# Performance work log

Measured on AMD Instinct MI355X. Metric: run time of the kernel, lower is better.

The kernel has to match this reference:

```python
import jax, jax.numpy as jnp
import numpy as np

B, T, C = 2, 2048, 1024
HS, DS = 8, 32      # short heads, short qk dim
HL, DL = 8, 128     # long heads, long qk dim
HD = 64             # value/output head dim = n_embd // n_head
WIN_S, WIN_L = 256, 1024
NEG = jnp.finfo(jnp.float32).min


def _window_mask(t, window):
    # additive mask: disallow future (i<j) and tokens older than the window
    i = jnp.arange(t)[:, None]
    j = jnp.arange(t)[None, :]
    bad = (i - j < 0) | (i - j >= window)
    return bad.astype(jnp.float32) * NEG  # [T,T]


def _attn(x, Wqk, Wv, n_h, d_qk, d_v, window):
    b, t, _ = x.shape
    qk = x @ Wqk                                      # [B,T,2*n_h*d_qk]
    q, k = jnp.split(qk, 2, axis=-1)
    q = q.reshape(b, t, n_h, d_qk).transpose(0, 2, 1, 3)  # [B,H,T,dqk]
    k = k.reshape(b, t, n_h, d_qk).transpose(0, 2, 1, 3)
    v = (x @ Wv).reshape(b, t, n_h, d_v).transpose(0, 2, 1, 3)  # [B,H,T,dv]
    scale = 1.0 / jnp.sqrt(jnp.float32(d_qk))
    scores = jnp.einsum('bhqd,bhkd->bhqk', q, k) * scale
    scores = scores + _window_mask(t, window)
    p = jax.nn.softmax(scores, axis=-1)
    return jnp.einsum('bhqk,bhkd->bhqd', p, v)        # [B,H,T,dv]


def setup_inputs() -> dict:
    key = jax.random.key(0)
    ks = jax.random.split(key, 6)
    s = 0.02
    return {
        'x': jax.random.normal(ks[0], (B, T, C), dtype=jnp.float32),
        'Wqk_short': jax.random.normal(ks[1], (C, 2 * HS * DS), dtype=jnp.float32) * s,
        'Wv_short': jax.random.normal(ks[2], (C, HS * HD), dtype=jnp.float32) * s,
        'Wqk_long': jax.random.normal(ks[3], (C, 2 * HL * DL), dtype=jnp.float32) * s,
        'Wv_long': jax.random.normal(ks[4], (C, HL * HD), dtype=jnp.float32) * s,
        'Wproj': jax.random.normal(ks[5], (C, C), dtype=jnp.float32) * s,
    }


def reference(x, Wqk_short, Wv_short, Wqk_long, Wv_long, Wproj):
    b, t, c = x.shape
    y_short = _attn(x, Wqk_short, Wv_short, HS, DS, HD, WIN_S)  # [B,HS,T,HD]
    y_long = _attn(x, Wqk_long, Wv_long, HL, DL, HD, WIN_L)     # [B,HL,T,HD]
    y = jnp.concatenate([y_short, y_long], axis=1)              # [B,H,T,HD]
    y = y.transpose(0, 2, 1, 3).reshape(b, t, c)
    return y @ Wproj
```

## Files before the change

kernel.cpp:

```cpp
#include <hip/hip_runtime.h>
#include <math.h>

#define B_    2
#define T_    2048
#define C_    1024
#define HS_   8
#define DS_   32
#define HL_   8
#define DL_   128
#define HD_   64
#define WINS_ 256
#define WINL_ 1024
#define NALL_ 3584

typedef __bf16 bf16x8 __attribute__((ext_vector_type(8)));
typedef float floatx4 __attribute__((ext_vector_type(4)));

__device__ __forceinline__ ushort f2bf(float f) {
    union { float f; unsigned u; } v; v.f = f;
    unsigned r = v.u + 0x7fff + ((v.u >> 16) & 1);
    return (ushort)(r >> 16);
}
__device__ __forceinline__ float bf2f(ushort u) {
    union { unsigned u; float f; } v; v.u = ((unsigned)u) << 16;
    return v.f;
}

#define DPP_STEP(x, ctrl, op)                                                \
    {                                                                        \
        float _t = __builtin_bit_cast(                                       \
            float, __builtin_amdgcn_update_dpp(                              \
                       0, __builtin_bit_cast(int, (x)), (ctrl), 0xf, 0xf,    \
                       true));                                               \
        (x) = op((x), _t);                                                   \
    }
__device__ __forceinline__ float dpp_max16(float x) {
    DPP_STEP(x, 0xB1, fmaxf);
    DPP_STEP(x, 0x4E, fmaxf);
    DPP_STEP(x, 0x141, fmaxf);
    DPP_STEP(x, 0x140, fmaxf);
    return x;
}
__device__ __forceinline__ float dpp_add16(float x) {
#define FADD_(a, b) ((a) + (b))
    DPP_STEP(x, 0xB1, FADD_);
    DPP_STEP(x, 0x4E, FADD_);
    DPP_STEP(x, 0x141, FADD_);
    DPP_STEP(x, 0x140, FADD_);
#undef FADD_
    return x;
}

__device__ __forceinline__ void gload_lds16(const void* g, void* l) {
    __builtin_amdgcn_global_load_lds(
        (const __attribute__((address_space(1))) void*)g,
        (__attribute__((address_space(3))) void*)l, 16, 0, 0);
}

__global__ __launch_bounds__(256) void prep(
    const float* __restrict__ x, ushort* __restrict__ x16,
    const float* __restrict__ Wqk_s, const float* __restrict__ Wv_s,
    const float* __restrict__ Wqk_l, const float* __restrict__ Wv_l,
    const float* __restrict__ Wproj, ushort* __restrict__ WallT,
    ushort* __restrict__ WprojT) {
    __shared__ float t[32][33];
    int bid = blockIdx.x;
    if (bid < 4096) {
        const int i = bid * 256 + threadIdx.x;
        float4 v = ((const float4*)x)[i];
        ushort4 o;
        o.x = f2bf(v.x); o.y = f2bf(v.y); o.z = f2bf(v.z); o.w = f2bf(v.w);
        ((ushort4*)x16)[i] = o;
        return;
    }
    bid -= 4096;
    const float* W; ushort* WT; int N, rowoff;
    if (bid < 512)       { W = Wqk_s; WT = WallT;  N = 512;  rowoff = 0; }
    else if (bid < 1024) { bid -= 512;  W = Wv_s;  WT = WallT;  N = 512;  rowoff = 512; }
    else if (bid < 3072) { bid -= 1024; W = Wqk_l; WT = WallT;  N = 2048; rowoff = 1024; }
    else if (bid < 3584) { bid -= 3072; W = Wv_l;  WT = WallT;  N = 512;  rowoff = 3072; }
    else                 { bid -= 3584; W = Wproj; WT = WprojT; N = 1024; rowoff = 0; }
    const int nt = N / 32;
    const int n0 = (bid % nt) * 32;
    const int k0 = (bid / nt) * 32;
    const int tx = threadIdx.x & 31;
    const int ty = threadIdx.x >> 5;
#pragma unroll
    for (int i = 0; i < 4; ++i)
        t[ty + 8 * i][tx] = W[(size_t)(k0 + ty + 8 * i) * N + n0 + tx];
    __syncthreads();
#pragma unroll
    for (int i = 0; i < 4; ++i)
        WT[(size_t)(rowoff + n0 + ty + 8 * i) * 1024 + k0 + tx] =
            f2bf(t[tx][ty + 8 * i]);
}

template <int BM, int BN, int TH, typename OT, bool FUSEV>
__global__ __launch_bounds__(TH, 4) void gemm_bf16(const ushort* __restrict__ A,
                                                   const ushort* __restrict__ BT,
                                                   OT* __restrict__ Cm,
                                                   ushort* __restrict__ VT,
                                                   int M, int N, int K) {
    __shared__ ushort S[3][(BM + BN) * 32];
    constexpr int WM = TH / 128;
    constexpr int NI = BM / WM / 16;
    constexpr int JB = BN / 32;
    constexpr int NLD = (BM + BN) * 4 / TH;

    const int tid = threadIdx.x;
    const int m0 = blockIdx.y * BM;
    const int n0 = blockIdx.x * BN;
    const int wave = tid >> 6;
    const int lane = tid & 63;
    const int wm = (wave >> 1) * (BM / WM);
    const int wn = (wave & 1) * (BN / 2);
    const int l15 = lane & 15;
    const int quad = lane >> 4;

    floatx4 acc[NI][JB] = {};

    const ushort* sbase[NLD];
#pragma unroll
    for (int i = 0; i < NLD; ++i) {
        const int idx = tid + TH * i;
        const int row = idx >> 2;
        const int ch = (idx & 3) * 8;
        sbase[i] = (row < BM) ? A + (size_t)(m0 + row) * K + ch
                              : BT + (size_t)(n0 + row - BM) * K + ch;
    }

#define STAGE(buf, kt)                                                      \
    {                                                                       \
        _Pragma("unroll") for (int i_ = 0; i_ < NLD; ++i_)                  \
            gload_lds16(sbase[i_] + (kt),                                   \
                        &S[buf][(wave * 64 + TH * i_) * 8]);                \
    }

#define COMPUTE(buf)                                                        \
    {                                                                       \
        bf16x8 af[NI], bfr[JB];                                             \
        _Pragma("unroll") for (int i = 0; i < NI; ++i) af[i] =              \
            *(const bf16x8*)&S[buf][(wm + i * 16 + l15) * 32 + quad * 8];   \
        _Pragma("unroll") for (int j = 0; j < JB; ++j) bfr[j] =             \
            *(const bf16x8*)&S[buf][(BM + wn + j * 16 + l15) * 32 +         \
                                    quad * 8];                              \
        _Pragma("unroll") for (int i = 0; i < NI; ++i)                      \
            _Pragma("unroll") for (int j = 0; j < JB; ++j) acc[i][j] =      \
                __builtin_amdgcn_mfma_f32_16x16x32_bf16(af[i], bfr[j],      \
                                                        acc[i][j], 0, 0, 0); \
    }

#define WAIT_CUR()                                                    \
    {                                                                 \
        if constexpr (NLD == 4)                                       \
            asm volatile("s_waitcnt vmcnt(4)" ::: "memory");          \
        else if constexpr (NLD == 3)                                  \
            asm volatile("s_waitcnt vmcnt(3)" ::: "memory");          \
        else                                                          \
            asm volatile("s_waitcnt vmcnt(2)" ::: "memory");          \
    }

    STAGE(0, 0);
    STAGE(1, 32);
    int cur = 0;
    for (int kt = 0; kt + 32 < K; kt += 32) {
        WAIT_CUR();
        __builtin_amdgcn_s_barrier();
        __builtin_amdgcn_sched_barrier(0);
        if (kt + 64 < K) {
            int nxt2 = cur + 2;
            if (nxt2 >= 3) nxt2 -= 3;
            STAGE(nxt2, kt + 64);
        }
        COMPUTE(cur);
        ++cur;
        if (cur == 3) cur = 0;
    }
    asm volatile("s_waitcnt vmcnt(0)" ::: "memory");
    __builtin_amdgcn_s_barrier();
    __builtin_amdgcn_sched_barrier(0);
    COMPUTE(cur);
#undef STAGE
#undef COMPUTE
#undef WAIT_CUR

    bool vtile = false;
    if constexpr (FUSEV)
        vtile = (n0 >= 512 && n0 < 1024) || (n0 >= 3072);

    if (FUSEV && vtile) {
#pragma unroll
        for (int i = 0; i < NI; ++i) {
            const int m = m0 + wm + i * 16 + quad * 4;
            const int bb = m >> 11;
            const int t = m & 2047;
#pragma unroll
            for (int j = 0; j < JB; ++j) {
                const int col = n0 + wn + j * 16 + l15;
                const int vcol = (col < 1024) ? (col - 512) : (col - 2560);
                ushort4 val;
                val.x = f2bf(acc[i][j][0]);
                val.y = f2bf(acc[i][j][1]);
                val.z = f2bf(acc[i][j][2]);
                val.w = f2bf(acc[i][j][3]);
                *(ushort4*)&VT[((size_t)(bb * 1024 + vcol)) * T_ + t] = val;
            }
        }
    } else {
#pragma unroll
        for (int i = 0; i < NI; ++i)
#pragma unroll
            for (int j = 0; j < JB; ++j)
#pragma unroll
                for (int r = 0; r < 4; ++r) {
                    const size_t idx =
                        (size_t)(m0 + wm + i * 16 + quad * 4 + r) * N + n0 +
                        wn + j * 16 + l15;
                    if constexpr (sizeof(OT) == 2)
                        Cm[idx] = f2bf(acc[i][j][r]);
                    else
                        Cm[idx] = acc[i][j][r];
                }
    }
}

template <int D, int WIN, bool SPLIT>
__device__ __forceinline__ void attn_dev(
    const ushort* __restrict__ act, const ushort* __restrict__ vt,
    ushort* __restrict__ y, ushort* __restrict__ po, float* __restrict__ pm,
    float* __restrict__ pl, float scale2, int qoff, int koff, int head_off,
    int h, int gh, int b, int t0, int zs, ushort* lds) {
    constexpr int STR = D + 8;
    constexpr int PSTR = 72;
    constexpr int NKS = D / 32;
    constexpr int QCH = D / 8;
    constexpr int NKLD = (64 * QCH) / 256;

    ushort* Ks = lds;
    ushort* VTs = Ks + 64 * STR;
    ushort* Ps = VTs + 64 * PSTR;

    const int tid = threadIdx.x;
    const int wave = tid >> 6;
    const int lane = tid & 63;
    const int l15 = lane & 15;
    const int quad = lane >> 4;
    const int qmin = t0 + wave * 16;

    int k0s = t0 - WIN + 1;
    if (k0s < 0) k0s = 0;
    k0s &= ~63;

    int ks_begin = k0s, ks_last = t0;
    if (SPLIT) {
        const int nt = ((t0 - k0s) >> 6) + 1;
        const int ntlo = (nt + 1) >> 1;
        if (zs == 0) {
            ks_last = k0s + (ntlo - 1) * 64;
        } else {
            if (ntlo >= nt) {
#pragma unroll
                for (int r = 0; r < 4; ++r) {
                    const int t = qmin + quad * 4 + r;
                    const size_t ridx =
                        (((size_t)(zs * 2 + b) * 8 + h) * T_ + t);
                    if (l15 == 0) { pm[ridx] = -1e30f; pl[ridx] = 0.f; }
#pragma unroll
                    for (int j = 0; j < 4; ++j)
                        po[ridx * 64 + j * 16 + l15] = 0;
                }
                return;
            }
            ks_begin = k0s + ntlo * 64;
        }
    }

    const ushort* qbase = act + (size_t)(b * T_ + t0) * NALL_ + qoff + h * D;
    const ushort* kbase = act + (size_t)(b * T_) * NALL_ + koff + h * D;
    const ushort* vtb = vt + (size_t)((b * 16 + gh) * HD_) * T_;

    int krow[NKLD], kch[NKLD];
#pragma unroll
    for (int i = 0; i < NKLD; ++i) {
        const int idx = tid + 256 * i;
        krow[i] = idx / QCH;
        kch[i] = idx % QCH;
    }
    const int vd0 = tid >> 3, vc0 = (tid & 7) * 8;
    const int vd1 = (tid + 256) >> 3, vc1 = ((tid + 256) & 7) * 8;

    int4 kreg[NKLD], vreg0, vreg1;
#pragma unroll
    for (int i = 0; i < NKLD; ++i)
        kreg[i] = *(const int4*)(kbase + (size_t)(ks_begin + krow[i]) * NALL_ +
                                 kch[i] * 8);
    vreg0 = *(const int4*)(vtb + (size_t)vd0 * T_ + ks_begin + vc0);
    vreg1 = *(const int4*)(vtb + (size_t)vd1 * T_ + ks_begin + vc1);

    for (int idx = tid; idx < 64 * QCH; idx += 256) {
        const int row = idx / QCH;
        const int ch = idx % QCH;
        *(int4*)&Ks[row * STR + ch * 8] =
            *(const int4*)(qbase + (size_t)row * NALL_ + ch * 8);
    }
    __syncthreads();
    bf16x8 qa[NKS];
#pragma unroll
    for (int ks = 0; ks < NKS; ++ks)
        qa[ks] = *(const bf16x8*)&Ks[(wave * 16 + l15) * STR + ks * 32 + quad * 8];

    float m_i[4], l_i[4];
    floatx4 o_acc[4] = {};
#pragma unroll
    for (int r = 0; r < 4; ++r) { m_i[r] = -1e30f; l_i[r] = 0.f; }

    for (int k0 = ks_begin; k0 <= ks_last; k0 += 64) {
        __syncthreads();
#pragma unroll
        for (int i = 0; i < NKLD; ++i)
            *(int4*)&Ks[krow[i] * STR + kch[i] * 8] = kreg[i];
        *(int4*)&VTs[vd0 * PSTR + vc0] = vreg0;
        *(int4*)&VTs[vd1 * PSTR + vc1] = vreg1;
        __syncthreads();
        if (k0 + 64 <= ks_last) {
#pragma unroll
            for (int i = 0; i < NKLD; ++i)
                kreg[i] = *(const int4*)(kbase +
                                         (size_t)(k0 + 64 + krow[i]) * NALL_ +
                                         kch[i] * 8);
            vreg0 = *(const int4*)(vtb + (size_t)vd0 * T_ + k0 + 64 + vc0);
            vreg1 = *(const int4*)(vtb + (size_t)vd1 * T_ + k0 + 64 + vc1);
        }

        floatx4 s[4] = {};
#pragma unroll
        for (int ks = 0; ks < NKS; ++ks) {
#pragma unroll
            for (int j = 0; j < 4; ++j) {
                const bf16x8 bb =
                    *(const bf16x8*)&Ks[(j * 16 + l15) * STR + ks * 32 + quad * 8];
                s[j] = __builtin_amdgcn_mfma_f32_16x16x32_bf16(qa[ks], bb, s[j],
                                                               0, 0, 0);
            }
        }

        const bool full = (k0 + 63 <= qmin) && ((qmin + 15) - k0 <= WIN - 1);
        if (full) {
#pragma unroll
            for (int j = 0; j < 4; ++j)
#pragma unroll
                for (int r = 0; r < 4; ++r) s[j][r] *= scale2;
        } else {
#pragma unroll
            for (int j = 0; j < 4; ++j) {
                const int kj = k0 + j * 16 + l15;
#pragma unroll
                for (int r = 0; r < 4; ++r) {
                    const int rel = (qmin + quad * 4 + r) - kj;
                    s[j][r] = (rel < 0 || rel >= WIN) ? -1e30f : s[j][r] * scale2;
                }
            }
        }

        float rm[4];
#pragma unroll
        for (int r = 0; r < 4; ++r) {
            float t = fmaxf(fmaxf(s[0][r], s[1][r]), fmaxf(s[2][r], s[3][r]));
            rm[r] = dpp_max16(t);
        }
        const bool need = (rm[0] > m_i[0] + 8.f) || (rm[1] > m_i[1] + 8.f) ||
                          (rm[2] > m_i[2] + 8.f) || (rm[3] > m_i[3] + 8.f);
        if (__any(need)) {
#pragma unroll
            for (int r = 0; r < 4; ++r) {
                const float mn = fmaxf(m_i[r], rm[r]);
                const float a = exp2f(m_i[r] - mn);
                m_i[r] = mn;
                l_i[r] *= a;
#pragma unroll
                for (int j = 0; j < 4; ++j) o_acc[j][r] *= a;
            }
        }
#pragma unroll
        for (int r = 0; r < 4; ++r) {
            float sum = 0.f;
#pragma unroll
            for (int j = 0; j < 4; ++j) {
                const float e = exp2f(s[j][r] - m_i[r]);
                sum += e;
                Ps[(wave * 16 + quad * 4 + r) * PSTR + j * 16 + l15] = f2bf(e);
            }
            sum = dpp_add16(sum);
            l_i[r] += sum;
        }

#pragma unroll
        for (int kks = 0; kks < 2; ++kks) {
            const bf16x8 pa =
                *(const bf16x8*)&Ps[(wave * 16 + l15) * PSTR + kks * 32 + quad * 8];
#pragma unroll
            for (int j = 0; j < 4; ++j) {
                const bf16x8 vb =
                    *(const bf16x8*)&VTs[(j * 16 + l15) * PSTR + kks * 32 + quad * 8];
                o_acc[j] = __builtin_amdgcn_mfma_f32_16x16x32_bf16(pa, vb, o_acc[j],
                                                                   0, 0, 0);
            }
        }
    }

    if (SPLIT) {
#pragma unroll
        for (int r = 0; r < 4; ++r) {
            const int t = qmin + quad * 4 + r;
            const size_t ridx = (((size_t)(zs * 2 + b) * 8 + h) * T_ + t);
            if (l15 == 0) { pm[ridx] = m_i[r]; pl[ridx] = l_i[r]; }
#pragma unroll
            for (int j = 0; j < 4; ++j)
                po[ridx * 64 + j * 16 + l15] = f2bf(o_acc[j][r]);
        }
    } else {
#pragma unroll
        for (int r = 0; r < 4; ++r) {
            const float inv = 1.f / l_i[r];
            ushort* yrow = y + (size_t)(b * T_ + qmin + quad * 4 + r) * C_ +
                           head_off + h * HD_;
#pragma unroll
            for (int j = 0; j < 4; ++j)
                yrow[j * 16 + l15] = f2bf(o_acc[j][r] * inv);
        }
    }
}

__global__ __launch_bounds__(256, 4) void attn_sched(
    const ushort* __restrict__ act, const ushort* __restrict__ vt,
    ushort* __restrict__ y, ushort* __restrict__ po, float* __restrict__ pm,
    float* __restrict__ pl) {
    extern __shared__ ushort smem[];
    int x = blockIdx.x;
    if (x < 1024) {
        const int zs = x & 1;
        const int b = (x >> 1) & 1;
        const int h = (x >> 2) & 7;
        const int t0 = (31 - (x >> 5)) * 64;
        attn_dev<DL_, WINL_, true>(act, vt, y, po, pm, pl,
                                   0.12752021352994164f,
                                   1024, 2048, 512, h, 8 + h, b, t0, zs, smem);
    } else {
        x -= 1024;
        const int b = x & 1;
        const int h = (x >> 1) & 7;
        const int t0 = (31 - (x >> 4)) * 64;
        attn_dev<DS_, WINS_, false>(act, vt, y, po, pm, pl,
                                    0.2550404270598833f,
                                    0, 256, 0, h, h, b, t0, 0, smem);
    }
}

__global__ __launch_bounds__(256) void combine(const ushort* __restrict__ po,
                                               const float* __restrict__ pm,
                                               const float* __restrict__ pl,
                                               ushort* __restrict__ y) {
    const int gid = blockIdx.x * 256 + threadIdx.x;
    const int row = gid >> 4;
    const int cg = (gid & 15) * 4;
    const int b = row >> 14;
    const int h = (row >> 11) & 7;
    const int t = row & 2047;

    const float m0 = pm[row], m1 = pm[32768 + row];
    const float l0 = pl[row], l1 = pl[32768 + row];
    const float m = fmaxf(m0, m1);
    const float e0 = exp2f(m0 - m);
    const float e1 = exp2f(m1 - m);
    const float inv = 1.f / (l0 * e0 + l1 * e1);

    const ushort4 o0 = *(const ushort4*)&po[(size_t)row * 64 + cg];
    const ushort4 o1 = *(const ushort4*)&po[((size_t)32768 + row) * 64 + cg];

    ushort4 r;
    r.x = f2bf((bf2f(o0.x) * e0 + bf2f(o1.x) * e1) * inv);
    r.y = f2bf((bf2f(o0.y) * e0 + bf2f(o1.y) * e1) * inv);
    r.z = f2bf((bf2f(o0.z) * e0 + bf2f(o1.z) * e1) * inv);
    r.w = f2bf((bf2f(o0.w) * e0 + bf2f(o1.w) * e1) * inv);
    *(ushort4*)&y[(size_t)(b * T_ + t) * C_ + 512 + h * 64 + cg] = r;
}

extern "C" void kernel_launch(void* const* d_in, const int* in_sizes, int n_in,
                              void* d_out, int out_size, void* d_ws,
                              size_t ws_size, hipStream_t stream) {
    const float* x         = (const float*)d_in[0];
    const float* Wqk_short = (const float*)d_in[1];
    const float* Wv_short  = (const float*)d_in[2];
    const float* Wqk_long  = (const float*)d_in[3];
    const float* Wv_long   = (const float*)d_in[4];
    const float* Wproj     = (const float*)d_in[5];
    float* out = (float*)d_out;

    const int M = B_ * T_;

    ushort* x16    = (ushort*)d_ws;
    ushort* WallT  = x16 + (size_t)M * C_;
    ushort* WprojT = WallT + (size_t)NALL_ * C_;
    ushort* yb16   = WprojT + (size_t)C_ * C_;
    ushort* act    = yb16 + (size_t)M * C_;
    ushort* vt     = act + (size_t)M * NALL_;
    ushort* po     = vt + (size_t)32 * HD_ * T_;
    float*  pm     = (float*)(po + (size_t)2 * 32768 * 64);
    float*  pl     = pm + (size_t)2 * 32768;

    dim3 blk(256);
    prep<<<dim3(8704), blk, 0, stream>>>(x, x16, Wqk_short, Wv_short, Wqk_long,
                                         Wv_long, Wproj, WallT, WprojT);

    gemm_bf16<256, 128, 512, ushort, true>
        <<<dim3(NALL_ / 128, M / 256), dim3(512), 0, stream>>>(
            x16, WallT, act, vt, M, NALL_, C_);

    const int attn_lds = (64 * (DL_ + 8) + 64 * 72 * 2) * 2;
    attn_sched<<<dim3(1536), blk, attn_lds, stream>>>(act, vt, yb16, po, pm, pl);

    combine<<<dim3(2048), blk, 0, stream>>>(po, pm, pl, yb16);

    gemm_bf16<64, 64, 256, float, false>
        <<<dim3(C_ / 64, M / 64), blk, 0, stream>>>(yb16, WprojT, out, nullptr,
                                                    M, C_, C_);
}
```

Before: 201.3 us.

## Use 128-query attention tiles with 8 waves sharing K/V loads

Each attention block now has 512 threads and covers 128 queries instead of 64, so every K/V tile staged in LDS is reused by twice as many waves and the grid is halved. Q fragments are now read straight from global memory into registers instead of being staged through LDS. The key range is extended by one tile to cover the larger query block. This raises per-block LDS and register demand and changes the split balance for the long heads.

```diff
diff --git a/kernel.cpp b/kernel.cpp
--- a/kernel.cpp
+++ b/kernel.cpp
@@ -231,14 +231,16 @@
     float* __restrict__ pl, float scale2, int qoff, int koff, int head_off,
     int h, int gh, int b, int t0, int zs, ushort* lds) {
     constexpr int STR = D + 8;
+    constexpr int VSTR = 72;
     constexpr int PSTR = 72;
     constexpr int NKS = D / 32;
     constexpr int QCH = D / 8;
-    constexpr int NKLD = (64 * QCH) / 256;
+    constexpr int KCH_TOT = 64 * QCH;
+    constexpr int NKLD = (KCH_TOT + 511) / 512;
 
     ushort* Ks = lds;
     ushort* VTs = Ks + 64 * STR;
-    ushort* Ps = VTs + 64 * PSTR;
+    ushort* Ps = VTs + 64 * VSTR;
 
     const int tid = threadIdx.x;
     const int wave = tid >> 6;
@@ -251,9 +253,9 @@
     if (k0s < 0) k0s = 0;
     k0s &= ~63;
 
-    int ks_begin = k0s, ks_last = t0;
+    int ks_begin = k0s, ks_last = t0 + 64;
     if (SPLIT) {
-        const int nt = ((t0 - k0s) >> 6) + 1;
+        const int nt = ((t0 + 64 - k0s) >> 6) + 1;
         const int ntlo = (nt + 1) >> 1;
         if (zs == 0) {
             ks_last = k0s + (ntlo - 1) * 64;
@@ -282,32 +284,26 @@
     int krow[NKLD], kch[NKLD];
 #pragma unroll
     for (int i = 0; i < NKLD; ++i) {
-        const int idx = tid + 256 * i;
+        const int idx = tid + 512 * i;
         krow[i] = idx / QCH;
         kch[i] = idx % QCH;
     }
-    const int vd0 = tid >> 3, vc0 = (tid & 7) * 8;
-    const int vd1 = (tid + 256) >> 3, vc1 = ((tid + 256) & 7) * 8;
-
-    int4 kreg[NKLD], vreg0, vreg1;
+    const int vd = tid >> 3, vc = (tid & 7) * 8;
+
+    int4 kreg[NKLD], vreg;
 #pragma unroll
     for (int i = 0; i < NKLD; ++i)
-        kreg[i] = *(const int4*)(kbase + (size_t)(ks_begin + krow[i]) * NALL_ +
-                                 kch[i] * 8);
-    vreg0 = *(const int4*)(vtb + (size_t)vd0 * T_ + ks_begin + vc0);
-    vreg1 = *(const int4*)(vtb + (size_t)vd1 * T_ + ks_begin + vc1);
-
-    for (int idx = tid; idx < 64 * QCH; idx += 256) {
-        const int row = idx / QCH;
-        const int ch = idx % QCH;
-        *(int4*)&Ks[row * STR + ch * 8] =
-            *(const int4*)(qbase + (size_t)row * NALL_ + ch * 8);
-    }
-    __syncthreads();
+        if (tid + 512 * i < KCH_TOT)
+            kreg[i] = *(const int4*)(kbase +
+                                     (size_t)(ks_begin + krow[i]) * NALL_ +
+                                     kch[i] * 8);
+    vreg = *(const int4*)(vtb + (size_t)vd * T_ + ks_begin + vc);
+
     bf16x8 qa[NKS];
 #pragma unroll
     for (int ks = 0; ks < NKS; ++ks)
-        qa[ks] = *(const bf16x8*)&Ks[(wave * 16 + l15) * STR + ks * 32 + quad * 8];
+        qa[ks] = *(const bf16x8*)(qbase + (size_t)(wave * 16 + l15) * NALL_ +
+                                  ks * 32 + quad * 8);
 
     float m_i[4], l_i[4];
     floatx4 o_acc[4] = {};
@@ -318,18 +314,19 @@
         __syncthreads();
 #pragma unroll
         for (int i = 0; i < NKLD; ++i)
-            *(int4*)&Ks[krow[i] * STR + kch[i] * 8] = kreg[i];
-        *(int4*)&VTs[vd0 * PSTR + vc0] = vreg0;
-        *(int4*)&VTs[vd1 * PSTR + vc1] = vreg1;
+            if (tid + 512 * i < KCH_TOT)
+                *(int4*)&Ks[krow[i] * STR + kch[i] * 8] = kreg[i];
+        *(int4*)&VTs[vd * VSTR + vc] = vreg;
         __syncthreads();
         if (k0 + 64 <= ks_last) {
 #pragma unroll
             for (int i = 0; i < NKLD; ++i)
-                kreg[i] = *(const int4*)(kbase +
-                                         (size_t)(k0 + 64 + krow[i]) * NALL_ +
-                                         kch[i] * 8);
-            vreg0 = *(const int4*)(vtb + (size_t)vd0 * T_ + k0 + 64 + vc0);
-            vreg1 = *(const int4*)(vtb + (size_t)vd1 * T_ + k0 + 64 + vc1);
+                if (tid + 512 * i < KCH_TOT)
+                    kreg[i] = *(const int4*)(kbase +
+                                             (size_t)(k0 + 64 + krow[i]) *
+                                                 NALL_ +
+                                             kch[i] * 8);
+            vreg = *(const int4*)(vtb + (size_t)vd * T_ + k0 + 64 + vc);
         }
 
         floatx4 s[4] = {};
@@ -401,7 +398,7 @@
 #pragma unroll
             for (int j = 0; j < 4; ++j) {
                 const bf16x8 vb =
-                    *(const bf16x8*)&VTs[(j * 16 + l15) * PSTR + kks * 32 + quad * 8];
+                    *(const bf16x8*)&VTs[(j * 16 + l15) * VSTR + kks * 32 + quad * 8];
                 o_acc[j] = __builtin_amdgcn_mfma_f32_16x16x32_bf16(pa, vb, o_acc[j],
                                                                    0, 0, 0);
             }
@@ -431,25 +428,25 @@
     }
 }
 
-__global__ __launch_bounds__(256, 4) void attn_sched(
+__global__ __launch_bounds__(512, 4) void attn_sched(
     const ushort* __restrict__ act, const ushort* __restrict__ vt,
     ushort* __restrict__ y, ushort* __restrict__ po, float* __restrict__ pm,
     float* __restrict__ pl) {
     extern __shared__ ushort smem[];
     int x = blockIdx.x;
-    if (x < 1024) {
+    if (x < 512) {
         const int zs = x & 1;
         const int b = (x >> 1) & 1;
         const int h = (x >> 2) & 7;
-        const int t0 = (31 - (x >> 5)) * 64;
+        const int t0 = (15 - (x >> 5)) * 128;
         attn_dev<DL_, WINL_, true>(act, vt, y, po, pm, pl,
                                    0.12752021352994164f,
                                    1024, 2048, 512, h, 8 + h, b, t0, zs, smem);
     } else {
-        x -= 1024;
+        x -= 512;
         const int b = x & 1;
         const int h = (x >> 1) & 7;
-        const int t0 = (31 - (x >> 4)) * 64;
+        const int t0 = (15 - (x >> 4)) * 128;
         attn_dev<DS_, WINS_, false>(act, vt, y, po, pm, pl,
                                     0.2550404270598833f,
                                     0, 256, 0, h, h, b, t0, 0, smem);
@@ -516,8 +513,9 @@
         <<<dim3(NALL_ / 128, M / 256), dim3(512), 0, stream>>>(
             x16, WallT, act, vt, M, NALL_, C_);
 
-    const int attn_lds = (64 * (DL_ + 8) + 64 * 72 * 2) * 2;
-    attn_sched<<<dim3(1536), blk, attn_lds, stream>>>(act, vt, yb16, po, pm, pl);
+    const int attn_lds = (64 * (DL_ + 8) + 64 * 72 + 128 * 72) * 2;
+    attn_sched<<<dim3(768), dim3(512), attn_lds, stream>>>(act, vt, yb16, po,
+                                                           pm, pl);
 
     combine<<<dim3(2048), blk, 0, stream>>>(po, pm, pl, yb16);
 
```

Result: faster. 192.9 us (median of 3 runs) (-4.2%).
